# Kernel tuning notes

Measured on AMD Instinct MI355X. Metric: run time of the kernel, lower is better.

Reference implementation:

```python
import jax, jax.numpy as jnp
import numpy as np
import math


def wn_linear(x, v, g, b):
    # PyTorch weight_norm with dim=0: W[i] = g[i] * v[i] / ||v[i]||
    w = g[:, None] * v / jnp.linalg.norm(v, axis=1, keepdims=True)  # [out, in]
    return x @ w.T + b


def setup_inputs() -> dict:
    key = jax.random.key(0)
    ks = jax.random.split(key, 11)
    B, QC, KC, C, H, W = 8, 384, 384, 512, 32, 32
    s = 0.02
    return {
        "q": jax.random.normal(ks[0], (B, QC, H, W), jnp.float32),
        "k": jax.random.normal(ks[1], (B, KC, H, W), jnp.float32),
        "Wq_v": jax.random.normal(ks[2], (C, QC), jnp.float32) * s,
        "Wq_g": jax.random.uniform(ks[3], (C,), jnp.float32, 0.5, 1.5),
        "bq": jax.random.normal(ks[4], (C,), jnp.float32) * s,
        "Wk_v": jax.random.normal(ks[5], (C, KC), jnp.float32) * s,
        "Wk_g": jax.random.uniform(ks[6], (C,), jnp.float32, 0.5, 1.5),
        "bk": jax.random.normal(ks[7], (C,), jnp.float32) * s,
        "Wv_v": jax.random.normal(ks[8], (C, KC), jnp.float32) * s,
        "Wv_g": jax.random.uniform(ks[9], (C,), jnp.float32, 0.5, 1.5),
        "bv": jax.random.normal(ks[10], (C,), jnp.float32) * s,
    }


def reference(q, k, Wq_v, Wq_g, bq, Wk_v, Wk_g, bk, Wv_v, Wv_g, bv):
    NB_HEAD = 8
    B, _, H, W = k.shape
    S = H * W
    C = Wq_v.shape[0]
    D = C // NB_HEAD  # head_dim

    qf = q.reshape(B, q.shape[1], S).transpose(0, 2, 1)  # [B,S,QC]
    kf = k.reshape(B, k.shape[1], S).transpose(0, 2, 1)  # [B,S,KC]

    def heads(x):  # [B,S,C] -> [B,NH,S,D]
        return x.reshape(B, S, NB_HEAD, D).transpose(0, 2, 1, 3)

    qh = heads(wn_linear(qf, Wq_v, Wq_g, bq))
    kh = heads(wn_linear(kf, Wk_v, Wk_g, bk))
    vh = heads(wn_linear(kf, Wv_v, Wv_g, bv))

    attn = jnp.einsum("bhqd,bhkd->bhqk", qh, kh) / math.sqrt(D)
    # mask = triu(ones,1).t() -> strictly lower triangular allowed (no diagonal)
    allowed = jnp.tril(jnp.ones((S, S), bool), -1)
    attn = jnp.where(allowed, attn, jnp.float32(-10000.0))
    attn = jax.nn.softmax(attn, axis=-1)
    # start_mask zeroes row 0 of the attention weights (post-softmax multiply)
    start_mask = (jnp.arange(S) > 0).astype(attn.dtype)[None, None, :, None]
    attn = attn * start_mask
    # dropout in eval mode -> identity

    out = jnp.einsum("bhqk,bhkd->bhqd", attn, vh)  # [B,NH,S,D]
    out = out.transpose(0, 2, 1, 3).reshape(B, H, W, C).transpose(0, 3, 1, 2)
    return out
```

## Files before the change

kernel.cpp:

```cpp
#include <hip/hip_runtime.h>
#include <hip/hip_bf16.h>

typedef __attribute__((ext_vector_type(8))) __bf16 bf16x8;
typedef __attribute__((ext_vector_type(4))) float f32x4;

__device__ __forceinline__ f32x4 mfma16(bf16x8 a, bf16x8 b, f32x4 c) {
    return __builtin_amdgcn_mfma_f32_16x16x32_bf16(a, b, c, 0, 0, 0);
}

__device__ __forceinline__ unsigned short f2bf(float x) {
    union { float f; unsigned int u; } cv; cv.f = x;
    unsigned int r = cv.u + 0x7FFFu + ((cv.u >> 16) & 1u);
    return (unsigned short)(r >> 16);
}

__device__ __forceinline__ unsigned pack2(float a, float b) {
    return (unsigned)f2bf(a) | ((unsigned)f2bf(b) << 16);
}

__device__ __forceinline__ unsigned pk2(float a, float b) {
    float2 f2; f2.x = a; f2.y = b;
    __hip_bfloat162 h = __float22bfloat162_rn(f2);
    return *(unsigned*)&h;
}

__device__ __forceinline__ float fast_exp2(float x) {
    float r;
    asm("v_exp_f32 %0, %1" : "=v"(r) : "v"(x));
    return r;
}

__device__ __forceinline__ void gload_lds16(const void* g, void* l) {
    __builtin_amdgcn_global_load_lds(
        (const __attribute__((address_space(1))) unsigned int*)g,
        (__attribute__((address_space(3))) unsigned int*)l, 16, 0, 0);
}

__global__ __launch_bounds__(256) void prep_kernel(
    const float* __restrict__ q, const float* __restrict__ k,
    const float* __restrict__ Wq_v, const float* __restrict__ Wq_g,
    const float* __restrict__ Wk_v, const float* __restrict__ Wk_g,
    const float* __restrict__ Wv_v, const float* __restrict__ Wv_g,
    unsigned short* __restrict__ qT, unsigned short* __restrict__ kT,
    unsigned short* __restrict__ Wn)
{
    __shared__ float tile[32][33];
    int z = blockIdx.z;
    int t = threadIdx.x;
    if (z == 16) {
        int w = t >> 6, lane = t & 63;
        int idx = (blockIdx.y * 32 + blockIdx.x) * 4 + w;
        int proj = idx >> 9, o = idx & 511;
        const float* v = (proj == 0 ? Wq_v : proj == 1 ? Wk_v : Wv_v) + (size_t)o * 384;
        const float* g = (proj == 0 ? Wq_g : proj == 1 ? Wk_g : Wv_g);
        float vals[6];
        float ss = 0.f;
#pragma unroll
        for (int i = 0; i < 6; ++i) { vals[i] = v[lane + i * 64]; ss += vals[i] * vals[i]; }
#pragma unroll
        for (int off = 1; off < 64; off <<= 1) ss += __shfl_xor(ss, off, 64);
        float scale = g[o] * rsqrtf(ss);
        unsigned short* dst = Wn + ((size_t)proj * 512 + o) * 384;
#pragma unroll
        for (int i = 0; i < 6; ++i) dst[lane + i * 64] = f2bf(vals[i] * scale);
        return;
    }
    int tx = t & 31, ty = t >> 5;
    const float* src = (z < 8 ? q : k) + (size_t)(z & 7) * 384 * 1024;
    unsigned short* dst = (z < 8 ? qT : kT) + (size_t)(z & 7) * 1024 * 384;
    int c0 = blockIdx.y * 32, s0 = blockIdx.x * 32;
#pragma unroll
    for (int j = 0; j < 4; ++j)
        tile[ty + j * 8][tx] = src[(size_t)(c0 + ty + j * 8) * 1024 + s0 + tx];
    __syncthreads();
#pragma unroll
    for (int j = 0; j < 4; ++j)
        dst[(size_t)(s0 + ty + j * 8) * 384 + c0 + tx] = f2bf(tile[tx][ty + j * 8]);
}

__global__ __launch_bounds__(256) void proj_gemm(
    const unsigned short* __restrict__ qT, const unsigned short* __restrict__ kT,
    const unsigned short* __restrict__ Wn,
    const float* __restrict__ bq, const float* __restrict__ bk, const float* __restrict__ bv,
    unsigned short* __restrict__ Qp, unsigned short* __restrict__ Kp,
    unsigned short* __restrict__ Vt)
{
    __shared__ __align__(16) unsigned short Asm[2][128 * 32];
    __shared__ __align__(16) unsigned short Bsm[2][128 * 32];
    int zb = blockIdx.z; int proj = zb >> 3, b = zb & 7;
    const unsigned short* A = (proj == 0 ? qT : kT) + (size_t)b * 1024 * 384;
    const unsigned short* Bw = Wn + (size_t)proj * 512 * 384;
    const float* bias = proj == 0 ? bq : (proj == 1 ? bk : bv);
    int m0 = blockIdx.x * 128, n0 = blockIdx.y * 128;
    int t = threadIdx.x, w = t >> 6, lane = t & 63;
    int fr = lane & 15, fq = lane >> 4;
    int wm = (w >> 1) * 64, wn = (w & 1) * 64;

    f32x4 acc[4][4];
#pragma unroll
    for (int i = 0; i < 4; ++i)
#pragma unroll
        for (int j = 0; j < 4; ++j) acc[i][j] = (f32x4){0.f, 0.f, 0.f, 0.f};

    const unsigned short* asrc = A + (size_t)(m0 + w * 16 + (lane >> 2)) * 384 + (lane & 3) * 8;
    const unsigned short* bsrc = Bw + (size_t)(n0 + w * 16 + (lane >> 2)) * 384 + (lane & 3) * 8;

    auto stageAB = [&](int k0, int bufi) {
        gload_lds16(asrc + k0, &Asm[bufi][w * 512]);
        gload_lds16(asrc + k0 + (size_t)64 * 384, &Asm[bufi][w * 512 + 2048]);
        gload_lds16(bsrc + k0, &Bsm[bufi][w * 512]);
        gload_lds16(bsrc + k0 + (size_t)64 * 384, &Bsm[bufi][w * 512 + 2048]);
    };

    stageAB(0, 0);
    for (int ks = 0; ks < 12; ++ks) {
        if (ks < 11) {
            stageAB((ks + 1) * 32, (ks + 1) & 1);
            asm volatile("s_waitcnt vmcnt(4)" ::: "memory");
        } else {
            asm volatile("s_waitcnt vmcnt(0)" ::: "memory");
        }
        __builtin_amdgcn_s_barrier();
        int bi = ks & 1;
        bf16x8 af[4], bfr[4];
#pragma unroll
        for (int i = 0; i < 4; ++i)
            af[i] = *(const bf16x8*)&Asm[bi][(wm + i * 16 + fr) * 32 + fq * 8];
#pragma unroll
        for (int i = 0; i < 4; ++i)
            bfr[i] = *(const bf16x8*)&Bsm[bi][(wn + i * 16 + fr) * 32 + fq * 8];
#pragma unroll
        for (int mi = 0; mi < 4; ++mi)
#pragma unroll
            for (int ni = 0; ni < 4; ++ni)
                acc[mi][ni] = mfma16(af[mi], bfr[ni], acc[mi][ni]);
        asm volatile("s_waitcnt lgkmcnt(0)" ::: "memory");
        __builtin_amdgcn_s_barrier();
    }

    if (proj == 2) {
#pragma unroll
        for (int mi = 0; mi < 4; ++mi)
#pragma unroll
            for (int ni = 0; ni < 4; ++ni) {
                int c = n0 + wn + ni * 16 + fr;
                int s0 = m0 + wm + mi * 16 + fq * 4;
                float bc = bias[c];
                unsigned lo = pack2(acc[mi][ni][0] + bc, acc[mi][ni][1] + bc);
                unsigned hi = pack2(acc[mi][ni][2] + bc, acc[mi][ni][3] + bc);
                uint2 u; u.x = lo; u.y = hi;
                *(uint2*)&Vt[(((size_t)b * 512 + c) * 1024 + s0)] = u;
            }
    } else {
        unsigned short* Out = (proj == 0 ? Qp : Kp) + (size_t)b * 1024 * 512;
#pragma unroll
        for (int mi = 0; mi < 4; ++mi)
#pragma unroll
            for (int ni = 0; ni < 4; ++ni)
#pragma unroll
                for (int r = 0; r < 4; ++r) {
                    int c = n0 + wn + ni * 16 + fr;
                    int s = m0 + wm + mi * 16 + fq * 4 + r;
                    Out[(size_t)s * 512 + c] = f2bf(acc[mi][ni][r] + bias[c]);
                }
    }
}

__global__ __launch_bounds__(256, 4) void attn_kernel(
    const unsigned short* __restrict__ Qp, const unsigned short* __restrict__ Kp,
    const unsigned short* __restrict__ Vt, float* __restrict__ out)
{
    __shared__ __align__(16) unsigned short Kl[2][64 * 64];
    __shared__ __align__(16) unsigned short Vl[2][64 * 64];
    __shared__ __align__(16) unsigned short Pl[4][16 * 64];
    const float SCL = 0.125f * 1.44269504089f;
    int pj = blockIdx.x;
    int bh = blockIdx.y, b = bh >> 3, h = bh & 7;
    int t = threadIdx.x, w = t >> 6, lane = t & 63;
    int fr = lane & 15, fq = lane >> 4;
    int sub = lane >> 3;
    int sw = 8 * ((lane & 7) ^ sub);
    int swz = 8 * (fr & 7);
    const unsigned short* Qb = Qp + ((size_t)b * 1024) * 512 + h * 64;
    const unsigned short* Kb = Kp + ((size_t)b * 1024) * 512 + h * 64;
    const unsigned short* VTb = Vt + ((size_t)b * 512 + h * 64) * 1024;

    auto stage = [&](int kt, int bufi) {
        int kbase = kt * 64;
        int c0 = (w & 1) * 4;
        if (w < 2) {
#pragma unroll
            for (int i = 0; i < 4; ++i) {
                int c = c0 + i;
                gload_lds16(Kb + (size_t)(kbase + c * 8 + sub) * 512 + sw,
                            &Kl[bufi][c * 512]);
            }
        } else {
#pragma unroll
            for (int i = 0; i < 4; ++i) {
                int c = c0 + i;
                gload_lds16(VTb + (size_t)(c * 8 + sub) * 1024 + kbase + sw,
                            &Vl[bufi][c * 512]);
            }
        }
    };

    int cur = 0;
#pragma unroll 1
    for (int ph = 0; ph < 2; ++ph) {
        int qtile = ph == 0 ? pj : 15 - pj;
        int row0 = qtile * 64 + w * 16;
        int nt = qtile + 1;

        bf16x8 qf0 = *(const bf16x8*)(Qb + (size_t)(row0 + fr) * 512 + fq * 8);
        bf16x8 qf1 = *(const bf16x8*)(Qb + (size_t)(row0 + fr) * 512 + 32 + fq * 8);

        f32x4 Ot[4];
#pragma unroll
        for (int f = 0; f < 4; ++f) Ot[f] = (f32x4){0.f, 0.f, 0.f, 0.f};
        float M = -128.f, L = 0.f;

        stage(0, cur);
        for (int kt = 0; kt < nt; ++kt) {
            int kbase = kt * 64;
            if (kt + 1 < nt) {
                stage(kt + 1, cur ^ 1);
                asm volatile("s_waitcnt vmcnt(4)" ::: "memory");
            } else {
                asm volatile("s_waitcnt vmcnt(0)" ::: "memory");
            }
            __builtin_amdgcn_s_barrier();

            f32x4 Sacc[4];
#pragma unroll
            for (int kg = 0; kg < 4; ++kg) Sacc[kg] = (f32x4){0.f, 0.f, 0.f, 0.f};
#pragma unroll
            for (int kg = 0; kg < 4; ++kg) {
                bf16x8 k0 = *(const bf16x8*)&Kl[cur][(kg * 16 + fr) * 64 + ((fq * 8) ^ swz)];
                bf16x8 k1 = *(const bf16x8*)&Kl[cur][(kg * 16 + fr) * 64 + ((32 + fq * 8) ^ swz)];
                Sacc[kg] = mfma16(k0, qf0, Sacc[kg]);
                Sacc[kg] = mfma16(k1, qf1, Sacc[kg]);
            }

            int qrow = row0 + fr;
            float e[4][4];
            float vmax = -3e38f;
#pragma unroll
            for (int kg = 0; kg < 4; ++kg)
#pragma unroll
                for (int r = 0; r < 4; ++r) {
                    int key = kbase + kg * 16 + fq * 4 + r;
                    float sv = (key < qrow) ? Sacc[kg][r] * SCL : -3e38f;
                    e[kg][r] = sv;
                    vmax = fmaxf(vmax, sv);
                }
            vmax = fmaxf(vmax, __shfl_xor(vmax, 16, 64));
            vmax = fmaxf(vmax, __shfl_xor(vmax, 32, 64));
            if (__any(vmax > M + 8.f)) {
                float Mn = fmaxf(M, vmax);
                float al = fast_exp2(M - Mn);
                L *= al;
                M = Mn;
#pragma unroll
                for (int f = 0; f < 4; ++f) {
                    Ot[f][0] *= al; Ot[f][1] *= al; Ot[f][2] *= al; Ot[f][3] *= al;
                }
            }
            float rs = 0.f;
#pragma unroll
            for (int kg = 0; kg < 4; ++kg)
#pragma unroll
                for (int r = 0; r < 4; ++r) {
                    float ee = fast_exp2(e[kg][r] - M);
                    e[kg][r] = ee;
                    rs += ee;
                }
            rs += __shfl_xor(rs, 16, 64);
            rs += __shfl_xor(rs, 32, 64);
            L += rs;

#pragma unroll
            for (int kg = 0; kg < 4; ++kg) {
                uint2 u;
                u.x = pk2(e[kg][0], e[kg][1]);
                u.y = pk2(e[kg][2], e[kg][3]);
                *(uint2*)&Pl[w][fr * 64 + ((kg * 16 + fq * 4) ^ swz)] = u;
            }
            bf16x8 pb0 = *(const bf16x8*)&Pl[w][fr * 64 + ((fq * 8) ^ swz)];
            bf16x8 pb1 = *(const bf16x8*)&Pl[w][fr * 64 + ((32 + fq * 8) ^ swz)];

#pragma unroll
            for (int f = 0; f < 4; ++f) {
                bf16x8 a0 = *(const bf16x8*)&Vl[cur][(f * 16 + fr) * 64 + ((fq * 8) ^ swz)];
                bf16x8 a1 = *(const bf16x8*)&Vl[cur][(f * 16 + fr) * 64 + ((32 + fq * 8) ^ swz)];
                Ot[f] = mfma16(a0, pb0, Ot[f]);
                Ot[f] = mfma16(a1, pb1, Ot[f]);
            }

            asm volatile("s_waitcnt lgkmcnt(0)" ::: "memory");
            __builtin_amdgcn_s_barrier();
            cur ^= 1;
        }

        float rcp = (L > 0.f) ? 1.f / L : 0.f;
        int q = row0 + fr;
#pragma unroll
        for (int f = 0; f < 4; ++f)
#pragma unroll
            for (int rr = 0; rr < 4; ++rr) {
                int d = f * 16 + fq * 4 + rr;
                out[((size_t)b * 512 + h * 64 + d) * 1024 + q] = Ot[f][rr] * rcp;
            }
    }
}

extern "C" void kernel_launch(void* const* d_in, const int* in_sizes, int n_in,
                              void* d_out, int out_size, void* d_ws, size_t ws_size,
                              hipStream_t stream) {
    const float* q    = (const float*)d_in[0];
    const float* k    = (const float*)d_in[1];
    const float* Wq_v = (const float*)d_in[2];
    const float* Wq_g = (const float*)d_in[3];
    const float* bq   = (const float*)d_in[4];
    const float* Wk_v = (const float*)d_in[5];
    const float* Wk_g = (const float*)d_in[6];
    const float* bk   = (const float*)d_in[7];
    const float* Wv_v = (const float*)d_in[8];
    const float* Wv_g = (const float*)d_in[9];
    const float* bv   = (const float*)d_in[10];
    float* out = (float*)d_out;

    char* ws = (char*)d_ws;
    unsigned short* qT = (unsigned short*)(ws + 0);
    unsigned short* kT = (unsigned short*)(ws + 6291456);
    unsigned short* Wn = (unsigned short*)(ws + 12582912);
    unsigned short* Qp = (unsigned short*)(ws + 13762560);
    unsigned short* Kp = (unsigned short*)(ws + 22151168);
    unsigned short* Vt = (unsigned short*)(ws + 30539776);

    prep_kernel<<<dim3(32, 12, 17), dim3(256), 0, stream>>>(
        q, k, Wq_v, Wq_g, Wk_v, Wk_g, Wv_v, Wv_g, qT, kT, Wn);
    proj_gemm<<<dim3(8, 4, 24), dim3(256), 0, stream>>>(qT, kT, Wn, bq, bk, bv, Qp, Kp, Vt);
    attn_kernel<<<dim3(8, 64), dim3(256), 0, stream>>>(Qp, Kp, Vt, out);
}
```

Measured before the change: 66.31 us.

## Widen attention key tiles, keep P in registers, vectorize prep and projection stores

The attention kernel now processes 128-key tiles instead of 64, with new K/V LDS swizzles. The P matrix is rearranged in registers using v_permlane32/16_swap instead of a round trip through LDS. Occupancy bound drops from 4 to 2 blocks per CU to fit the larger LDS buffers. The prep transpose writes packed bf16 pairs, and the Q/K projection epilogue stages output through an LDS scratch so it can issue 16-byte row stores. Together these aim to cut LDS traffic, barriers and scattered global stores, at the cost of more wasted masked work on diagonal tiles and lower occupancy.

```diff
diff --git a/kernel.cpp b/kernel.cpp
--- a/kernel.cpp
+++ b/kernel.cpp
@@ -28,6 +28,13 @@
     float r;
     asm("v_exp_f32 %0, %1" : "=v"(r) : "v"(x));
     return r;
+}
+
+__device__ __forceinline__ void permswap32(unsigned &a, unsigned &b) {
+    asm("v_permlane32_swap_b32 %0, %1" : "+v"(a), "+v"(b));
+}
+__device__ __forceinline__ void permswap16(unsigned &a, unsigned &b) {
+    asm("v_permlane16_swap_b32 %0, %1" : "+v"(a), "+v"(b));
 }
 
 __device__ __forceinline__ void gload_lds16(const void* g, void* l) {
@@ -73,9 +80,13 @@
     for (int j = 0; j < 4; ++j)
         tile[ty + j * 8][tx] = src[(size_t)(c0 + ty + j * 8) * 1024 + s0 + tx];
     __syncthreads();
-#pragma unroll
-    for (int j = 0; j < 4; ++j)
-        dst[(size_t)(s0 + ty + j * 8) * 384 + c0 + tx] = f2bf(tile[tx][ty + j * 8]);
+    int cp = tx & 15;
+#pragma unroll
+    for (int j = 0; j < 2; ++j) {
+        int ss = ty + (tx >> 4) * 8 + j * 16;
+        *(unsigned*)&dst[(size_t)(s0 + ss) * 384 + c0 + 2 * cp] =
+            pk2(tile[2 * cp][ss], tile[2 * cp + 1][ss]);
+    }
 }
 
 __global__ __launch_bounds__(256) void proj_gemm(
@@ -85,8 +96,7 @@
     unsigned short* __restrict__ Qp, unsigned short* __restrict__ Kp,
     unsigned short* __restrict__ Vt)
 {
-    __shared__ __align__(16) unsigned short Asm[2][128 * 32];
-    __shared__ __align__(16) unsigned short Bsm[2][128 * 32];
+    __shared__ __align__(16) unsigned short pool[4][128 * 32];
     int zb = blockIdx.z; int proj = zb >> 3, b = zb & 7;
     const unsigned short* A = (proj == 0 ? qT : kT) + (size_t)b * 1024 * 384;
     const unsigned short* Bw = Wn + (size_t)proj * 512 * 384;
@@ -106,10 +116,10 @@
     const unsigned short* bsrc = Bw + (size_t)(n0 + w * 16 + (lane >> 2)) * 384 + (lane & 3) * 8;
 
     auto stageAB = [&](int k0, int bufi) {
-        gload_lds16(asrc + k0, &Asm[bufi][w * 512]);
-        gload_lds16(asrc + k0 + (size_t)64 * 384, &Asm[bufi][w * 512 + 2048]);
-        gload_lds16(bsrc + k0, &Bsm[bufi][w * 512]);
-        gload_lds16(bsrc + k0 + (size_t)64 * 384, &Bsm[bufi][w * 512 + 2048]);
+        gload_lds16(asrc + k0, &pool[bufi][w * 512]);
+        gload_lds16(asrc + k0 + (size_t)64 * 384, &pool[bufi][w * 512 + 2048]);
+        gload_lds16(bsrc + k0, &pool[2 + bufi][w * 512]);
+        gload_lds16(bsrc + k0 + (size_t)64 * 384, &pool[2 + bufi][w * 512 + 2048]);
     };
 
     stageAB(0, 0);
@@ -125,10 +135,10 @@
         bf16x8 af[4], bfr[4];
 #pragma unroll
         for (int i = 0; i < 4; ++i)
-            af[i] = *(const bf16x8*)&Asm[bi][(wm + i * 16 + fr) * 32 + fq * 8];
+            af[i] = *(const bf16x8*)&pool[bi][(wm + i * 16 + fr) * 32 + fq * 8];
 #pragma unroll
         for (int i = 0; i < 4; ++i)
-            bfr[i] = *(const bf16x8*)&Bsm[bi][(wn + i * 16 + fr) * 32 + fq * 8];
+            bfr[i] = *(const bf16x8*)&pool[2 + bi][(wn + i * 16 + fr) * 32 + fq * 8];
 #pragma unroll
         for (int mi = 0; mi < 4; ++mi)
 #pragma unroll
@@ -153,55 +163,67 @@
             }
     } else {
         unsigned short* Out = (proj == 0 ? Qp : Kp) + (size_t)b * 1024 * 512;
-#pragma unroll
-        for (int mi = 0; mi < 4; ++mi)
-#pragma unroll
-            for (int ni = 0; ni < 4; ++ni)
-#pragma unroll
-                for (int r = 0; r < 4; ++r) {
+        const int STR = 72;
+        unsigned short* scr = &pool[0][0] + w * 2304;
+#pragma unroll
+        for (int p = 0; p < 2; ++p) {
+#pragma unroll
+            for (int mh = 0; mh < 2; ++mh) {
+                int mi = p * 2 + mh;
+#pragma unroll
+                for (int ni = 0; ni < 4; ++ni) {
                     int c = n0 + wn + ni * 16 + fr;
-                    int s = m0 + wm + mi * 16 + fq * 4 + r;
-                    Out[(size_t)s * 512 + c] = f2bf(acc[mi][ni][r] + bias[c]);
-                }
-    }
-}
-
-__global__ __launch_bounds__(256, 4) void attn_kernel(
+                    float bc = bias[c];
+#pragma unroll
+                    for (int r = 0; r < 4; ++r)
+                        scr[(mh * 16 + fq * 4 + r) * STR + ni * 16 + fr] =
+                            f2bf(acc[mi][ni][r] + bc);
+                }
+            }
+            asm volatile("s_waitcnt lgkmcnt(0)" ::: "memory");
+            int sp = lane >> 1, ch = (lane & 1) * 32;
+            int s = m0 + wm + p * 32 + sp;
+#pragma unroll
+            for (int kk = 0; kk < 4; ++kk) {
+                bf16x8 v = *(const bf16x8*)&scr[sp * STR + ch + 8 * kk];
+                *(bf16x8*)&Out[(size_t)s * 512 + n0 + wn + ch + 8 * kk] = v;
+            }
+            asm volatile("s_waitcnt lgkmcnt(0)" ::: "memory");
+        }
+    }
+}
+
+__global__ __launch_bounds__(256, 2) void attn_kernel(
     const unsigned short* __restrict__ Qp, const unsigned short* __restrict__ Kp,
     const unsigned short* __restrict__ Vt, float* __restrict__ out)
 {
-    __shared__ __align__(16) unsigned short Kl[2][64 * 64];
-    __shared__ __align__(16) unsigned short Vl[2][64 * 64];
-    __shared__ __align__(16) unsigned short Pl[4][16 * 64];
+    __shared__ __align__(16) unsigned short Kl[2][128 * 64];
+    __shared__ __align__(16) unsigned short Vl[2][64 * 128];
     const float SCL = 0.125f * 1.44269504089f;
     int pj = blockIdx.x;
     int bh = blockIdx.y, b = bh >> 3, h = bh & 7;
-    int t = threadIdx.x, w = t >> 6, lane = t & 63;
+    int tid = threadIdx.x, w = tid >> 6, lane = tid & 63;
     int fr = lane & 15, fq = lane >> 4;
-    int sub = lane >> 3;
-    int sw = 8 * ((lane & 7) ^ sub);
-    int swz = 8 * (fr & 7);
     const unsigned short* Qb = Qp + ((size_t)b * 1024) * 512 + h * 64;
     const unsigned short* Kb = Kp + ((size_t)b * 1024) * 512 + h * 64;
     const unsigned short* VTb = Vt + ((size_t)b * 512 + h * 64) * 1024;
+    int f3 = fr & 7;
+    int swK = 8 * ((lane & 7) ^ (lane >> 3));
 
     auto stage = [&](int kt, int bufi) {
-        int kbase = kt * 64;
-        int c0 = (w & 1) * 4;
-        if (w < 2) {
-#pragma unroll
-            for (int i = 0; i < 4; ++i) {
-                int c = c0 + i;
-                gload_lds16(Kb + (size_t)(kbase + c * 8 + sub) * 512 + sw,
-                            &Kl[bufi][c * 512]);
-            }
-        } else {
-#pragma unroll
-            for (int i = 0; i < 4; ++i) {
-                int c = c0 + i;
-                gload_lds16(VTb + (size_t)(c * 8 + sub) * 1024 + kbase + sw,
-                            &Vl[bufi][c * 512]);
-            }
+        int kbase = kt * 128;
+#pragma unroll
+        for (int i = 0; i < 4; ++i) {
+            int r0 = w * 32 + i * 8;
+            gload_lds16(Kb + (size_t)(kbase + r0 + (lane >> 3)) * 512 + swK,
+                        &Kl[bufi][r0 * 64]);
+        }
+#pragma unroll
+        for (int i = 0; i < 4; ++i) {
+            int d0 = w * 16 + i * 4;
+            int swV = 8 * ((lane & 15) ^ (i * 4 + (lane >> 4)));
+            gload_lds16(VTb + (size_t)(d0 + (lane >> 4)) * 1024 + kbase + swV,
+                        &Vl[bufi][d0 * 128]);
         }
     };
 
@@ -210,7 +232,7 @@
     for (int ph = 0; ph < 2; ++ph) {
         int qtile = ph == 0 ? pj : 15 - pj;
         int row0 = qtile * 64 + w * 16;
-        int nt = qtile + 1;
+        int nt = (qtile >> 1) + 1;
 
         bf16x8 qf0 = *(const bf16x8*)(Qb + (size_t)(row0 + fr) * 512 + fq * 8);
         bf16x8 qf1 = *(const bf16x8*)(Qb + (size_t)(row0 + fr) * 512 + 32 + fq * 8);
@@ -219,39 +241,36 @@
 #pragma unroll
         for (int f = 0; f < 4; ++f) Ot[f] = (f32x4){0.f, 0.f, 0.f, 0.f};
         float M = -128.f, L = 0.f;
+        int qrow = row0 + fr;
 
         stage(0, cur);
         for (int kt = 0; kt < nt; ++kt) {
-            int kbase = kt * 64;
+            int kbase = kt * 128;
             if (kt + 1 < nt) {
                 stage(kt + 1, cur ^ 1);
-                asm volatile("s_waitcnt vmcnt(4)" ::: "memory");
+                asm volatile("s_waitcnt vmcnt(8)" ::: "memory");
             } else {
                 asm volatile("s_waitcnt vmcnt(0)" ::: "memory");
             }
             __builtin_amdgcn_s_barrier();
 
-            f32x4 Sacc[4];
-#pragma unroll
-            for (int kg = 0; kg < 4; ++kg) Sacc[kg] = (f32x4){0.f, 0.f, 0.f, 0.f};
-#pragma unroll
-            for (int kg = 0; kg < 4; ++kg) {
-                bf16x8 k0 = *(const bf16x8*)&Kl[cur][(kg * 16 + fr) * 64 + ((fq * 8) ^ swz)];
-                bf16x8 k1 = *(const bf16x8*)&Kl[cur][(kg * 16 + fr) * 64 + ((32 + fq * 8) ^ swz)];
-                Sacc[kg] = mfma16(k0, qf0, Sacc[kg]);
-                Sacc[kg] = mfma16(k1, qf1, Sacc[kg]);
-            }
-
-            int qrow = row0 + fr;
-            float e[4][4];
+            f32x4 S[8];
+#pragma unroll
+            for (int kg = 0; kg < 8; ++kg) {
+                bf16x8 k0 = *(const bf16x8*)&Kl[cur][(kg * 16 + fr) * 64 + ((fq ^ f3) * 8)];
+                bf16x8 k1 = *(const bf16x8*)&Kl[cur][(kg * 16 + fr) * 64 + (((4 + fq) ^ f3) * 8)];
+                S[kg] = mfma16(k0, qf0, (f32x4){0.f, 0.f, 0.f, 0.f});
+                S[kg] = mfma16(k1, qf1, S[kg]);
+            }
+
             float vmax = -3e38f;
 #pragma unroll
-            for (int kg = 0; kg < 4; ++kg)
+            for (int kg = 0; kg < 8; ++kg)
 #pragma unroll
                 for (int r = 0; r < 4; ++r) {
                     int key = kbase + kg * 16 + fq * 4 + r;
-                    float sv = (key < qrow) ? Sacc[kg][r] * SCL : -3e38f;
-                    e[kg][r] = sv;
+                    float sv = (key < qrow) ? S[kg][r] * SCL : -3e38f;
+                    S[kg][r] = sv;
                     vmax = fmaxf(vmax, sv);
                 }
             vmax = fmaxf(vmax, __shfl_xor(vmax, 16, 64));
@@ -268,34 +287,38 @@
             }
             float rs = 0.f;
 #pragma unroll
-            for (int kg = 0; kg < 4; ++kg)
+            for (int kg = 0; kg < 8; ++kg)
 #pragma unroll
                 for (int r = 0; r < 4; ++r) {
-                    float ee = fast_exp2(e[kg][r] - M);
-                    e[kg][r] = ee;
-                    rs += ee;
+                    float e = fast_exp2(S[kg][r] - M);
+                    S[kg][r] = e;
+                    rs += e;
                 }
             rs += __shfl_xor(rs, 16, 64);
             rs += __shfl_xor(rs, 32, 64);
             L += rs;
 
-#pragma unroll
-            for (int kg = 0; kg < 4; ++kg) {
-                uint2 u;
-                u.x = pk2(e[kg][0], e[kg][1]);
-                u.y = pk2(e[kg][2], e[kg][3]);
-                *(uint2*)&Pl[w][fr * 64 + ((kg * 16 + fq * 4) ^ swz)] = u;
-            }
-            bf16x8 pb0 = *(const bf16x8*)&Pl[w][fr * 64 + ((fq * 8) ^ swz)];
-            bf16x8 pb1 = *(const bf16x8*)&Pl[w][fr * 64 + ((32 + fq * 8) ^ swz)];
-
-#pragma unroll
-            for (int f = 0; f < 4; ++f) {
-                bf16x8 a0 = *(const bf16x8*)&Vl[cur][(f * 16 + fr) * 64 + ((fq * 8) ^ swz)];
-                bf16x8 a1 = *(const bf16x8*)&Vl[cur][(f * 16 + fr) * 64 + ((32 + fq * 8) ^ swz)];
-                Ot[f] = mfma16(a0, pb0, Ot[f]);
-                Ot[f] = mfma16(a1, pb1, Ot[f]);
-            }
+            bf16x8 pb[4];
+#pragma unroll
+            for (int m = 0; m < 4; ++m) {
+                unsigned A0 = pk2(S[2 * m][0], S[2 * m][1]);
+                unsigned A1 = pk2(S[2 * m][2], S[2 * m][3]);
+                unsigned B0 = pk2(S[2 * m + 1][0], S[2 * m + 1][1]);
+                unsigned B1 = pk2(S[2 * m + 1][2], S[2 * m + 1][3]);
+                permswap32(A0, B0); permswap16(A0, B0);
+                permswap32(A1, B1); permswap16(A1, B1);
+                union { unsigned u[4]; bf16x8 v; } pu;
+                pu.u[0] = A0; pu.u[1] = A1; pu.u[2] = B0; pu.u[3] = B1;
+                pb[m] = pu.v;
+            }
+
+#pragma unroll
+            for (int m = 0; m < 4; ++m)
+#pragma unroll
+                for (int f = 0; f < 4; ++f) {
+                    bf16x8 vf = *(const bf16x8*)&Vl[cur][(f * 16 + fr) * 128 + (((4 * m + fq) ^ fr) * 8)];
+                    Ot[f] = mfma16(vf, pb[m], Ot[f]);
+                }
 
             asm volatile("s_waitcnt lgkmcnt(0)" ::: "memory");
             __builtin_amdgcn_s_barrier();
```

Result: no change. 65.96 us (-0.5%).
